# Kernel optimization log

Hardware: AMD Instinct MI355X
Metric: run time of the kernel (lower is better)

Reference implementation:

```python
import jax, jax.numpy as jnp
import numpy as np

DIM = 1024
D_INNER = 2048

def setup_inputs() -> dict:
    key = jax.random.key(0)
    ks = jax.random.split(key, 8)
    B, T = 8, 1024
    x = jax.random.normal(ks[0], (B, T, DIM), dtype=jnp.float32)
    h0 = jnp.zeros((B, D_INNER), dtype=jnp.float32)
    # params (xavier-ish scales)
    in_proj_w = jax.random.normal(ks[1], (D_INNER, DIM), dtype=jnp.float32) * (2.0 / (DIM + D_INNER)) ** 0.5
    out_proj_w = jax.random.normal(ks[2], (DIM, D_INNER), dtype=jnp.float32) * (2.0 / (DIM + D_INNER)) ** 0.5
    c_h = jax.random.uniform(ks[3], (D_INNER,), jnp.float32, -0.1, 0.1)
    # spectral normalization as in _init_weights
    c_h = c_h * jnp.minimum(1.0, 0.99 / jnp.abs(jnp.fft.fft(c_h)).max())
    c_x = jax.random.uniform(ks[4], (D_INNER,), jnp.float32, -0.1, 0.1)
    c_x = c_x * jnp.minimum(1.0, 0.99 / jnp.abs(jnp.fft.fft(c_x)).max())
    b = jnp.zeros((D_INNER,), dtype=jnp.float32)
    W_gate = jax.random.normal(ks[5], (D_INNER, D_INNER), dtype=jnp.float32) * (1.0 / D_INNER) ** 0.5
    b_gate = jnp.zeros((D_INNER,), dtype=jnp.float32)
    return {"x": x, "h0": h0, "in_proj_w": in_proj_w, "out_proj_w": out_proj_w,
            "c_h": c_h, "c_x": c_x, "b": b, "W_gate": W_gate, "b_gate": b_gate}

def _circ_apply_fft(fft_c, v):
    # circ(c) @ v along last axis via real FFT; v: [..., D]
    D = v.shape[-1]
    return jnp.fft.irfft(fft_c * jnp.fft.rfft(v, axis=-1), n=D, axis=-1)

def reference(x, h0, in_proj_w, out_proj_w, c_h, c_x, b, W_gate, b_gate):
    B, T, _ = x.shape
    D = h0.shape[-1]
    x_proj = jnp.einsum('btd,ed->bte', x, in_proj_w)  # [B,T,D_inner]
    # gate path (fully parallel over T)
    gate = jax.nn.silu(jnp.einsum('bte,fe->btf', x_proj, W_gate) + b_gate)
    # input circulant contribution, parallel over all tokens
    pre = _circ_apply_fft(jnp.fft.rfft(c_x), x_proj) + b  # [B,T,D]
    fft_ch = jnp.fft.rfft(c_h)

    def step(h_prev, pre_t):
        h_new = jnp.tanh(_circ_apply_fft(fft_ch, h_prev) + pre_t)
        return h_new, h_new

    pre_tbd = jnp.transpose(pre, (1, 0, 2))  # [T,B,D]
    h_final, h_seq = jax.lax.scan(step, h0, pre_tbd)  # h_seq: [T,B,D]
    cell_out = jnp.transpose(h_seq, (1, 0, 2)) * gate  # [B,T,D]
    output = jnp.einsum('bte,de->btd', cell_out, out_proj_w)  # [B,T,dim]
    return output, h_final
```

## Files before the change

kernel.cpp:

```cpp
#include <hip/hip_runtime.h>
#include <cstdint>
#include <cstddef>

#define DI 2048
#define DM 1024
#define BB 8
#define TT 1024
#define ROWS (BB*TT)
#define NSCAN 32

typedef short  short8 __attribute__((ext_vector_type(8)));
typedef float  f32x4  __attribute__((ext_vector_type(4)));

__device__ __forceinline__ unsigned short f2bf(float f) {
  unsigned int u = __builtin_bit_cast(unsigned int, f);
  u = u + 0x7fffu + ((u >> 16) & 1u);
  return (unsigned short)(u >> 16);
}
__device__ __forceinline__ float fast_tanh(float x) {
  float ax = fabsf(x);
  float e  = __expf(-2.0f * ax);
  float t  = (1.0f - e) / (1.0f + e);
  return x < 0.0f ? -t : t;
}
__device__ __forceinline__ float silu_f(float z) {
  return z / (1.0f + __expf(-z));
}
__device__ __forceinline__ unsigned mulpk(unsigned a, unsigned b) {
  float a0 = __builtin_bit_cast(float, a << 16);
  float a1 = __builtin_bit_cast(float, a & 0xffff0000u);
  float b0 = __builtin_bit_cast(float, b << 16);
  float b1 = __builtin_bit_cast(float, b & 0xffff0000u);
  unsigned r0 = f2bf(a0 * b0), r1 = f2bf(a1 * b1);
  return r0 | (r1 << 16);
}
__device__ __forceinline__ uint4 pack8(const unsigned short* q) {
  uint4 p;
  p.x = (unsigned)q[0] | ((unsigned)q[1] << 16);
  p.y = (unsigned)q[2] | ((unsigned)q[3] << 16);
  p.z = (unsigned)q[4] | ((unsigned)q[5] << 16);
  p.w = (unsigned)q[6] | ((unsigned)q[7] << 16);
  return p;
}

__global__ void cast_k(const float* __restrict__ s, short* __restrict__ d, int n4) {
  int i = blockIdx.x * 256 + threadIdx.x;
  if (i >= n4) return;
  float4 f = ((const float4*)s)[i];
  unsigned lo = (unsigned)f2bf(f.x) | ((unsigned)f2bf(f.y) << 16);
  unsigned hi = (unsigned)f2bf(f.z) | ((unsigned)f2bf(f.w) << 16);
  uint2 o; o.x = lo; o.y = hi;
  ((uint2*)d)[i] = o;
}

__global__ void build_cx_k(const float* __restrict__ cx, short* __restrict__ C) {
  int tid = blockIdx.x * 256 + threadIdx.x;
  int n   = tid >> 8;
  int k0  = (tid & 255) * 8;
  unsigned short q[8];
#pragma unroll
  for (int j = 0; j < 8; ++j) q[j] = f2bf(cx[(n - (k0 + j)) & (DI - 1)]);
  *(uint4*)(C + (size_t)n * DI + k0) = pack8(q);
}

__global__ __launch_bounds__(256) void gemm_k(
    const short* __restrict__ A, const short* __restrict__ A2,
    const short* __restrict__ Bt,
    int M, int N, int K, int mode, const float* __restrict__ bias,
    float* __restrict__ outF, short* __restrict__ outH)
{
  __shared__ __align__(16) short As[128 * 40];
  __shared__ __align__(16) short Bs[128 * 40];
  const int tid  = threadIdx.x;
  const int m0   = blockIdx.y * 128, n0 = blockIdx.x * 128;
  const int wave = tid >> 6, lane = tid & 63;
  const int wy = wave >> 1, wx = wave & 1;
  const int l = lane & 15, G = lane >> 4;
  const int srow = tid >> 1, sseg = tid & 1;

  f32x4 acc[4][4];
#pragma unroll
  for (int i = 0; i < 4; ++i)
#pragma unroll
    for (int j = 0; j < 4; ++j) acc[i][j] = (f32x4){0.f, 0.f, 0.f, 0.f};

  for (int k0 = 0; k0 < K; k0 += 32) {
    if (k0) __syncthreads();
    const short* ga = A  + (size_t)(m0 + srow) * K + k0 + sseg * 16;
    const short* gb = Bt + (size_t)(n0 + srow) * K + k0 + sseg * 16;
    uint4 a0 = *(const uint4*)ga;
    uint4 a1 = *(const uint4*)(ga + 8);
    if (A2) {
      const short* g2 = A2 + (size_t)(m0 + srow) * K + k0 + sseg * 16;
      uint4 m0v = *(const uint4*)g2;
      uint4 m1v = *(const uint4*)(g2 + 8);
      a0.x = mulpk(a0.x, m0v.x); a0.y = mulpk(a0.y, m0v.y);
      a0.z = mulpk(a0.z, m0v.z); a0.w = mulpk(a0.w, m0v.w);
      a1.x = mulpk(a1.x, m1v.x); a1.y = mulpk(a1.y, m1v.y);
      a1.z = mulpk(a1.z, m1v.z); a1.w = mulpk(a1.w, m1v.w);
    }
    uint4 b0 = *(const uint4*)gb;
    uint4 b1 = *(const uint4*)(gb + 8);
    *(uint4*)&As[srow * 40 + sseg * 16]     = a0;
    *(uint4*)&As[srow * 40 + sseg * 16 + 8] = a1;
    *(uint4*)&Bs[srow * 40 + sseg * 16]     = b0;
    *(uint4*)&Bs[srow * 40 + sseg * 16 + 8] = b1;
    __syncthreads();
    short8 af[4], bfv[4];
#pragma unroll
    for (int i = 0; i < 4; ++i) af[i]  = *(const short8*)&As[(64 * wy + 16 * i + l) * 40 + 8 * G];
#pragma unroll
    for (int j = 0; j < 4; ++j) bfv[j] = *(const short8*)&Bs[(64 * wx + 16 * j + l) * 40 + 8 * G];
#pragma unroll
    for (int i = 0; i < 4; ++i)
#pragma unroll
      for (int j = 0; j < 4; ++j)
        acc[i][j] = __builtin_amdgcn_mfma_f32_16x16x32_bf16(af[i], bfv[j], acc[i][j], 0, 0, 0);
  }

#pragma unroll
  for (int j = 0; j < 4; ++j) {
    const int c = n0 + 64 * wx + 16 * j + l;
    float bv = 0.f;
    if (mode == 1 || mode == 2) bv = bias[c];
#pragma unroll
    for (int i = 0; i < 4; ++i) {
      const int r0 = m0 + 64 * wy + 16 * i + 4 * G;
#pragma unroll
      for (int v = 0; v < 4; ++v) {
        float z = acc[i][j][v] + bv;
        size_t off = (size_t)(r0 + v) * N + c;
        if (mode == 0)      outH[off] = (short)f2bf(z);
        else if (mode == 2) outH[off] = (short)f2bf(silu_f(z));
        else                outF[off] = z;
      }
    }
  }
}

__global__ __launch_bounds__(512, 2) void fused_k(
    const float* __restrict__ pre, const float* __restrict__ h0,
    const float* __restrict__ ch, short* __restrict__ hseq,
    float* __restrict__ hfin,
    const short* __restrict__ xproj, const short* __restrict__ wg,
    const float* __restrict__ bg, short* __restrict__ gate,
    unsigned* __restrict__ flags)
{
  __shared__ __align__(16) char smem[86016];
  const int bid = blockIdx.x;
  const int tid = threadIdx.x;

  if (bid < NSCAN) {
    short* h_lds = (short*)smem;
    float* part  = (float*)(smem + 4096);
    const int b = bid >> 2, c = bid & 3;
    const int w = tid >> 6, lane = tid & 63;
    const int q = lane & 15, G = lane >> 4;
    const float* preB = pre + (size_t)b * TT * DI + 512 * c;
    unsigned* myflag = flags + (4 * b + c) * 32;

    short8 av[16];
#pragma unroll
    for (int idx = 0; idx < 16; ++idx) {
      const int base = 16 * (idx - 14) + q - 8 * G - 256 * w;
      short8 v;
#pragma unroll
      for (int j = 0; j < 8; ++j)
        v[j] = (short)f2bf(ch[(base - j) & (DI - 1)]);
      av[idx] = v;
    }

    {
      float4 hv = *(const float4*)(h0 + b * DI + 4 * tid);
      unsigned lo = (unsigned)f2bf(hv.x) | ((unsigned)f2bf(hv.y) << 16);
      unsigned hi = (unsigned)f2bf(hv.z) | ((unsigned)f2bf(hv.w) << 16);
      const int blk = tid >> 1;
      const int pb  = blk ^ ((blk >> 4) & 7);
      uint2 wv; wv.x = lo; wv.y = hi;
      *(uint2*)&h_lds[pb * 8 + 4 * (tid & 1)] = wv;
    }
    float pcur = preB[tid];

    const int bbase = 64 * c + 32 * w + 4 * q + G;

    for (int t = 0; t < TT; ++t) {
      if (t) {
        const int pc = (lane < 3) ? (lane + (lane >= c ? 1 : 0)) : 0;
        const unsigned* fp = flags + (4 * b + pc) * 32;
        while (true) {
          unsigned v = __hip_atomic_load(fp, __ATOMIC_RELAXED, __HIP_MEMORY_SCOPE_AGENT);
          bool ok = (lane < 3) ? (v >= (unsigned)t) : true;
          if (__all(ok)) break;
          __builtin_amdgcn_s_sleep(2);
        }
        const unsigned* rowU = (const unsigned*)(hseq + (size_t)(b * TT + t - 1) * DI);
        unsigned d0 = __hip_atomic_load(rowU + tid,       __ATOMIC_RELAXED, __HIP_MEMORY_SCOPE_AGENT);
        unsigned d1 = __hip_atomic_load(rowU + tid + 512, __ATOMIC_RELAXED, __HIP_MEMORY_SCOPE_AGENT);
        const int blkA = tid >> 2,        pbA = blkA ^ ((blkA >> 4) & 7);
        const int blkB = (tid + 512) >> 2, pbB = blkB ^ ((blkB >> 4) & 7);
        *(unsigned*)&h_lds[pbA * 8 + 2 * (tid & 3)] = d0;
        *(unsigned*)&h_lds[pbB * 8 + 2 * (tid & 3)] = d1;
      }
      __syncthreads();

      float pf = preB[(size_t)(t + 1 < TT ? t + 1 : t) * DI + tid];

      f32x4 acc0 = (f32x4){0.f, 0.f, 0.f, 0.f};
      f32x4 acc1 = (f32x4){0.f, 0.f, 0.f, 0.f};
#pragma unroll
      for (int s = 0; s < 8; ++s) {
        const int blk = (bbase + 4 * s) & 255;
        const int pb  = blk ^ ((blk >> 4) & 7);
        short8 bv = *(const short8*)&h_lds[pb * 8];
        acc0 = __builtin_amdgcn_mfma_f32_16x16x32_bf16(av[14 - 2 * s], bv, acc0, 0, 0, 0);
        acc1 = __builtin_amdgcn_mfma_f32_16x16x32_bf16(av[15 - 2 * s], bv, acc1, 0, 0, 0);
      }
      {
        float* pk = part + (w << 9);
        const int f0 = 8 * q + G,     p0 = f0 ^ ((f0 >> 4) & 7);
        const int f1 = 8 * q + 4 + G, p1 = f1 ^ ((f1 >> 4) & 7);
        *(f32x4*)&pk[4 * p0] = acc0;
        *(f32x4*)&pk[4 * p1] = acc1;
      }
      __syncthreads();

      {
        const int f = tid >> 2, vv = tid & 3;
        const int pfz = f ^ ((f >> 4) & 7);
        const int off = 4 * pfz + vv;
        float z = ((part[off] + part[512 + off]) + (part[1024 + off] + part[1536 + off]))
                + ((part[2048 + off] + part[2560 + off]) + (part[3072 + off] + part[3584 + off]))
                + pcur;
        float th = fast_tanh(z);
        unsigned hv = (unsigned)f2bf(th);
        unsigned other = (unsigned)__shfl_xor((int)hv, 1);
        if (!(lane & 1)) {
          unsigned dw = (hv & 0xffffu) | (other << 16);
          unsigned* rowO = (unsigned*)(hseq + (size_t)(b * TT + t) * DI);
          __hip_atomic_store(rowO + 256 * c + (tid >> 1), dw,
                             __ATOMIC_RELAXED, __HIP_MEMORY_SCOPE_AGENT);
        }
        if (t == TT - 1) hfin[b * DI + 512 * c + tid] = th;
      }
      __syncthreads();
      if (tid == 0)
        __hip_atomic_store(myflag, (unsigned)(t + 1),
                           __ATOMIC_RELAXED, __HIP_MEMORY_SCOPE_AGENT);
      pcur = pf;
    }
  } else {
    short* As = (short*)smem;
    short* Bs = (short*)(smem + 20480);
    const int wid = tid >> 6, lane = tid & 63;
    const int wy = wid >> 1, wx = wid & 1;
    const int l = lane & 15, G = lane >> 4;

    for (int tile = bid - NSCAN; tile < 512; tile += (256 - NSCAN)) {
      const int m0 = (tile & 31) * 256, n0 = (tile >> 5) * 128;
      f32x4 acc[4][4];
#pragma unroll
      for (int i = 0; i < 4; ++i)
#pragma unroll
        for (int j = 0; j < 4; ++j) acc[i][j] = (f32x4){0.f, 0.f, 0.f, 0.f};

      for (int k0 = 0; k0 < DI; k0 += 32) {
        __syncthreads();
        const short* ga = xproj + (size_t)(m0 + (tid >> 1)) * DI + k0 + (tid & 1) * 16;
        const short* gb = wg    + (size_t)(n0 + (tid >> 2)) * DI + k0 + (tid & 3) * 8;
        uint4 a0 = *(const uint4*)ga;
        uint4 a1 = *(const uint4*)(ga + 8);
        uint4 b0 = *(const uint4*)gb;
        *(uint4*)&As[(tid >> 1) * 40 + (tid & 1) * 16]     = a0;
        *(uint4*)&As[(tid >> 1) * 40 + (tid & 1) * 16 + 8] = a1;
        *(uint4*)&Bs[(tid >> 2) * 40 + (tid & 3) * 8]      = b0;
        __syncthreads();
        short8 af[4], bfv[4];
#pragma unroll
        for (int i = 0; i < 4; ++i) af[i]  = *(const short8*)&As[(64 * wy + 16 * i + l) * 40 + 8 * G];
#pragma unroll
        for (int j = 0; j < 4; ++j) bfv[j] = *(const short8*)&Bs[(64 * wx + 16 * j + l) * 40 + 8 * G];
#pragma unroll
        for (int i = 0; i < 4; ++i)
#pragma unroll
          for (int j = 0; j < 4; ++j)
            acc[i][j] = __builtin_amdgcn_mfma_f32_16x16x32_bf16(af[i], bfv[j], acc[i][j], 0, 0, 0);
      }
#pragma unroll
      for (int j = 0; j < 4; ++j) {
        const int cidx = n0 + 64 * wx + 16 * j + l;
        const float bv = bg[cidx];
#pragma unroll
        for (int i = 0; i < 4; ++i) {
          const int r0 = m0 + 64 * wy + 16 * i + 4 * G;
#pragma unroll
          for (int v = 0; v < 4; ++v) {
            float z = acc[i][j][v] + bv;
            gate[(size_t)(r0 + v) * DI + cidx] = (short)f2bf(silu_f(z));
          }
        }
      }
      __syncthreads();
    }
  }
}

extern "C" void kernel_launch(void* const* d_in, const int* in_sizes, int n_in,
                              void* d_out, int out_size, void* d_ws, size_t ws_size,
                              hipStream_t stream) {
  const float* x    = (const float*)d_in[0];
  const float* h0   = (const float*)d_in[1];
  const float* win  = (const float*)d_in[2];
  const float* wout = (const float*)d_in[3];
  const float* ch   = (const float*)d_in[4];
  const float* cx   = (const float*)d_in[5];
  const float* bb   = (const float*)d_in[6];
  const float* wg   = (const float*)d_in[7];
  const float* bg   = (const float*)d_in[8];
  float* out = (float*)d_out;

  char* ws = (char*)d_ws;
  short* o_xb    = (short*)(ws + 0);
  short* o_win   = (short*)(ws + 16777216);
  short* o_cx    = (short*)(ws + 20971520);
  short* o_hseq  = (short*)(ws + 0);
  short* o_xproj = (short*)(ws + 33554432);
  float* o_pre   = (float*)(ws + 67108864);
  short* o_wout  = (short*)(ws + 67108864);
  short* o_gate  = (short*)(ws + 134217728);
  short* o_wg    = (short*)(ws + 167772160);

  cast_k<<<8192, 256, 0, stream>>>(x,   o_xb,  (BB * TT * DM) / 4);
  cast_k<<<2048, 256, 0, stream>>>(win, o_win, (DI * DM) / 4);
  cast_k<<<4096, 256, 0, stream>>>(wg,  o_wg,  (DI * DI) / 4);
  build_cx_k<<<2048, 256, 0, stream>>>(cx, o_cx);

  gemm_k<<<dim3(DI / 128, ROWS / 128), 256, 0, stream>>>(
      o_xb, nullptr, o_win, ROWS, DI, DM, 0, nullptr, nullptr, o_xproj);

  gemm_k<<<dim3(DI / 128, ROWS / 128), 256, 0, stream>>>(
      o_xproj, nullptr, o_cx, ROWS, DI, DI, 1, bb, o_pre, nullptr);

  hipMemsetAsync(d_out, 0, 4096, stream);

  fused_k<<<256, 512, 0, stream>>>(o_pre, h0, ch, o_hseq,
                                   out + (size_t)BB * TT * DM,
                                   o_xproj, o_wg, bg, o_gate,
                                   (unsigned*)d_out);

  cast_k<<<2048, 256, 0, stream>>>(wout, o_wout, (DM * DI) / 4);

  gemm_k<<<dim3(DM / 128, ROWS / 128), 256, 0, stream>>>(
      o_hseq, o_gate, o_wout, ROWS, DM, DI, 3, nullptr, out, nullptr);
}
```

Before: 2.222 ms.

## Replace flag-based scan sync with self-validating tagged packet exchange

The recurrent scan blocks stop publishing a per-step flag and polling it before reading the hidden row from global memory. Each block now writes 16-byte packets that carry two words of its new hidden slice plus the step index, using cache-bypassing stores into a double-buffered exchange area. Consumers spin on the packet itself until the tag matches, and the block's own slice is written straight to LDS. This removes one barrier and the flag round trip per step. It relies on a 16-byte store being seen atomically, on the double buffer not being overwritten early, and on the buffer being memset to 0xFF beforehand.

```diff
diff --git a/kernel.cpp b/kernel.cpp
--- a/kernel.cpp
+++ b/kernel.cpp
@@ -11,6 +11,7 @@
 
 typedef short  short8 __attribute__((ext_vector_type(8)));
 typedef float  f32x4  __attribute__((ext_vector_type(4)));
+typedef unsigned u32x4 __attribute__((ext_vector_type(4)));
 
 __device__ __forceinline__ unsigned short f2bf(float f) {
   unsigned int u = __builtin_bit_cast(unsigned int, f);
@@ -41,6 +42,17 @@
   p.z = (unsigned)q[4] | ((unsigned)q[5] << 16);
   p.w = (unsigned)q[6] | ((unsigned)q[7] << 16);
   return p;
+}
+
+__device__ __forceinline__ u32x4 ld_packet(const void* p) {
+  u32x4 r;
+  asm volatile("global_load_dwordx4 %0, %1, off sc0 sc1\n\ts_waitcnt vmcnt(0)"
+               : "=v"(r) : "v"(p) : "memory");
+  return r;
+}
+__device__ __forceinline__ void st_packet(void* p, u32x4 v) {
+  asm volatile("global_store_dwordx4 %0, %1, off sc0 sc1"
+               :: "v"(p), "v"(v) : "memory");
 }
 
 __global__ void cast_k(const float* __restrict__ s, short* __restrict__ d, int n4) {
@@ -144,7 +156,7 @@
     float* __restrict__ hfin,
     const short* __restrict__ xproj, const short* __restrict__ wg,
     const float* __restrict__ bg, short* __restrict__ gate,
-    unsigned* __restrict__ flags)
+    u32x4* __restrict__ exbuf)
 {
   __shared__ __align__(16) char smem[86016];
   const int bid = blockIdx.x;
@@ -157,7 +169,6 @@
     const int w = tid >> 6, lane = tid & 63;
     const int q = lane & 15, G = lane >> 4;
     const float* preB = pre + (size_t)b * TT * DI + 512 * c;
-    unsigned* myflag = flags + (4 * b + c) * 32;
 
     short8 av[16];
 #pragma unroll
@@ -184,26 +195,21 @@
     const int bbase = 64 * c + 32 * w + 4 * q + G;
 
     for (int t = 0; t < TT; ++t) {
-      if (t) {
-        const int pc = (lane < 3) ? (lane + (lane >= c ? 1 : 0)) : 0;
-        const unsigned* fp = flags + (4 * b + pc) * 32;
-        while (true) {
-          unsigned v = __hip_atomic_load(fp, __ATOMIC_RELAXED, __HIP_MEMORY_SCOPE_AGENT);
-          bool ok = (lane < 3) ? (v >= (unsigned)t) : true;
-          if (__all(ok)) break;
-          __builtin_amdgcn_s_sleep(2);
-        }
-        const unsigned* rowU = (const unsigned*)(hseq + (size_t)(b * TT + t - 1) * DI);
-        unsigned d0 = __hip_atomic_load(rowU + tid,       __ATOMIC_RELAXED, __HIP_MEMORY_SCOPE_AGENT);
-        unsigned d1 = __hip_atomic_load(rowU + tid + 512, __ATOMIC_RELAXED, __HIP_MEMORY_SCOPE_AGENT);
-        const int blkA = tid >> 2,        pbA = blkA ^ ((blkA >> 4) & 7);
-        const int blkB = (tid + 512) >> 2, pbB = blkB ^ ((blkB >> 4) & 7);
-        *(unsigned*)&h_lds[pbA * 8 + 2 * (tid & 3)] = d0;
-        *(unsigned*)&h_lds[pbB * 8 + 2 * (tid & 3)] = d1;
+      float pf = preB[(size_t)(t + 1 < TT ? t + 1 : t) * DI + tid];
+
+      if (t && tid < 384) {
+        const int pci = tid >> 7;
+        const int pc  = pci + (pci >= c ? 1 : 0);
+        const int p   = tid & 127;
+        u32x4* addr = exbuf + ((size_t)(((t - 1) & 1) * BB + b) * 4 + pc) * 128 + p;
+        u32x4 pkt;
+        do { pkt = ld_packet(addr); } while (pkt[2] != (unsigned)(t - 1));
+        const int n   = 512 * pc + 4 * p;
+        const int blk = n >> 3, pb = blk ^ ((blk >> 4) & 7);
+        uint2 wv; wv.x = pkt[0]; wv.y = pkt[1];
+        *(uint2*)&h_lds[pb * 8 + 4 * (p & 1)] = wv;
       }
       __syncthreads();
-
-      float pf = preB[(size_t)(t + 1 < TT ? t + 1 : t) * DI + tid];
 
       f32x4 acc0 = (f32x4){0.f, 0.f, 0.f, 0.f};
       f32x4 acc1 = (f32x4){0.f, 0.f, 0.f, 0.f};
@@ -232,20 +238,24 @@
                 + ((part[2048 + off] + part[2560 + off]) + (part[3072 + off] + part[3584 + off]))
                 + pcur;
         float th = fast_tanh(z);
-        unsigned hv = (unsigned)f2bf(th);
-        unsigned other = (unsigned)__shfl_xor((int)hv, 1);
+        unsigned hvu = (unsigned)f2bf(th);
+        unsigned o1  = (unsigned)__shfl_xor((int)hvu, 1);
+        unsigned dw  = (hvu & 0xffffu) | (o1 << 16);
+        unsigned dw2 = (unsigned)__shfl_xor((int)dw, 2);
+        if (t < TT - 1 && (lane & 3) == 0) {
+          u32x4 pkt; pkt[0] = dw; pkt[1] = dw2; pkt[2] = (unsigned)t; pkt[3] = 0u;
+          u32x4* addr = exbuf + ((size_t)((t & 1) * BB + b) * 4 + c) * 128 + (tid >> 2);
+          st_packet(addr, pkt);
+        }
         if (!(lane & 1)) {
-          unsigned dw = (hv & 0xffffu) | (other << 16);
+          const int n   = 512 * c + tid;
+          const int blk = n >> 3, pb = blk ^ ((blk >> 4) & 7);
+          *(unsigned*)&h_lds[pb * 8 + (n & 6)] = dw;
           unsigned* rowO = (unsigned*)(hseq + (size_t)(b * TT + t) * DI);
-          __hip_atomic_store(rowO + 256 * c + (tid >> 1), dw,
-                             __ATOMIC_RELAXED, __HIP_MEMORY_SCOPE_AGENT);
+          rowO[256 * c + (tid >> 1)] = dw;
         }
         if (t == TT - 1) hfin[b * DI + 512 * c + tid] = th;
       }
-      __syncthreads();
-      if (tid == 0)
-        __hip_atomic_store(myflag, (unsigned)(t + 1),
-                           __ATOMIC_RELAXED, __HIP_MEMORY_SCOPE_AGENT);
       pcur = pf;
     }
   } else {
@@ -340,12 +350,12 @@
   gemm_k<<<dim3(DI / 128, ROWS / 128), 256, 0, stream>>>(
       o_xproj, nullptr, o_cx, ROWS, DI, DI, 1, bb, o_pre, nullptr);
 
-  hipMemsetAsync(d_out, 0, 4096, stream);
+  hipMemsetAsync(d_out, 0xFF, 2 * BB * 4 * 128 * 16, stream);
 
   fused_k<<<256, 512, 0, stream>>>(o_pre, h0, ch, o_hseq,
                                    out + (size_t)BB * TT * DM,
                                    o_xproj, o_wg, bg, o_gate,
-                                   (unsigned*)d_out);
+                                   (u32x4*)d_out);
 
   cast_k<<<2048, 256, 0, stream>>>(wout, o_wout, (DM * DI) / 4);
 
```

After: 2.058 ms. -7.4%, faster.
